# Performance work log

Hardware: AMD Instinct MI355X
Metric: run time of the kernel (lower is better)

The kernel has to match this reference:

```python
import jax, jax.numpy as jnp
import numpy as np

B, T = 65536, 100          # batch of trajectories, hard-coded 100-step unrolled loop
D_CP, D_FIN, HID, D_OUT = 2, 3, 12, 2  # control-point dim, finger dim, SimpleRNN units, Dense out


def setup_inputs() -> dict:
    key = jax.random.key(0)
    k0, k1, k2, k3, k4 = jax.random.split(key, 5)
    return {
        "control_point_input": jax.random.normal(k0, (B, T, D_CP), jnp.float32),
        "finger_input": jax.random.normal(k1, (B, T, D_FIN), jnp.float32),
        # SimpleRNN kernel / recurrent kernel / bias ('random_normal', 'zeros')
        "W_rnn": jax.random.normal(k2, (D_CP + D_FIN, HID), jnp.float32) * 0.05,
        "U_rnn": jax.random.normal(k3, (HID, HID), jnp.float32) * 0.05,
        "b_rnn": jnp.zeros((HID,), jnp.float32),
        # Dense(2) kernel / bias
        "W_out": jax.random.normal(k4, (D_CP + HID, D_OUT), jnp.float32) * 0.05,
        "b_out": jnp.zeros((D_OUT,), jnp.float32),
    }


def reference(control_point_input, finger_input, W_rnn, U_rnn, b_rnn, W_out, b_out):
    """Non-teacher-forcing branch of DeformationTrackerBiFlowModel.call.

    Keras SimpleRNN (stateful=False) is invoked on a single timestep each
    iteration, so its hidden state is reset to zero every call and the
    recurrent kernel U_rnn contributes h0 @ U_rnn == 0 (mathematically inert).
    The true autoregressive recurrence flows through the Dense(2) output fed
    back as the next step's input -> expressed with a single lax.scan.
    """
    cp0 = control_point_input[:, 0, :]                # (B, 2), reused at every step
    fin = jnp.transpose(finger_input, (1, 0, 2))      # (T, B, 3) for scan

    def step(prev_out, fin_t):
        # prev_out: (B, 2) previous predicted control point; fin_t: (B, 3)
        x = jnp.concatenate([prev_out, fin_t], axis=-1)          # (B, 5)
        h = jnp.tanh(x @ W_rnn + b_rnn)                          # (B, 12); h0 @ U_rnn == 0
        out = jnp.concatenate([cp0, h], axis=-1) @ W_out + b_out  # (B, 2)
        return out, out

    _, outs = jax.lax.scan(step, cp0, fin)            # outs: (T, B, 2)
    return jnp.transpose(outs, (1, 0, 2))             # (B, T, 2)
```

## Files before the change

kernel.cpp:

```cpp
#include <hip/hip_runtime.h>


constexpr int Bn  = 65536;
constexpr int Tn  = 100;
constexpr int HID = 12;
constexpr int LPR = 4;
constexpr int UPL = 3;

template <int CTRL>
__device__ __forceinline__ float dpp_mov(float x) {
    return __builtin_bit_cast(float,
        __builtin_amdgcn_mov_dpp(__builtin_bit_cast(int, x), CTRL, 0xF, 0xF, true));
}

__device__ __forceinline__ float fast_tanh(float a) {
    const float t = __builtin_amdgcn_exp2f(a * 2.885390081777927f);
    return __builtin_fmaf(-2.0f, __builtin_amdgcn_rcpf(1.0f + t), 1.0f);
}

__global__ __launch_bounds__(256, 4) void deform_kernel(
    const float* __restrict__ cp,
    const float* __restrict__ fin,
    const float* __restrict__ Wr,
    const float* __restrict__ br_,
    const float* __restrict__ Wo,
    const float* __restrict__ bo_,
    float* __restrict__ out)
{
    const int tid = blockIdx.x * blockDim.x + threadIdx.x;
    const int row = tid >> 2;
    const int q   = tid & 3;
    const int j0  = q * UPL;

    float w0[UPL], w1[UPL], w2[UPL], w3[UPL], w4[UPL];
    float brv[UPL], wo0[UPL], wo1[UPL];
    #pragma unroll
    for (int u = 0; u < UPL; ++u) {
        const int j = j0 + u;
        w0[u] = Wr[0 * HID + j];
        w1[u] = Wr[1 * HID + j];
        w2[u] = Wr[2 * HID + j];
        w3[u] = Wr[3 * HID + j];
        w4[u] = Wr[4 * HID + j];
        brv[u] = br_[j];
        wo0[u] = Wo[(2 + j) * 2 + 0];
        wo1[u] = Wo[(2 + j) * 2 + 1];
    }
    const float wo00 = Wo[0], wo01 = Wo[1];
    const float wo10 = Wo[2], wo11 = Wo[3];
    const float bo0 = bo_[0], bo1 = bo_[1];

    const float cp0x = cp[(size_t)row * Tn * 2 + 0];
    const float cp0y = cp[(size_t)row * Tn * 2 + 1];

    const float oc0 = bo0 + cp0x * wo00 + cp0y * wo10;
    const float oc1 = bo1 + cp0x * wo01 + cp0y * wo11;

    float px = cp0x, py = cp0y;

    const float4* __restrict__ fp = reinterpret_cast<const float4*>(fin + (size_t)row * Tn * 3);
    float2* __restrict__ op = reinterpret_cast<float2*>(out + (size_t)row * Tn * 2);

    float4 cur0 = fp[0], cur1 = fp[1], cur2 = fp[2];
    float4 nxt0 = fp[3], nxt1 = fp[4], nxt2 = fp[5];

    #pragma unroll 1
    for (int c = 0; c < 25; ++c) {
        const int cpre = (c + 2 < 25) ? (c + 2) : 24;
        const float4 pf0 = fp[cpre * 3 + 0];
        const float4 pf1 = fp[cpre * 3 + 1];
        const float4 pf2 = fp[cpre * 3 + 2];

        const float f[12] = {cur0.x, cur0.y, cur0.z, cur0.w,
                             cur1.x, cur1.y, cur1.z, cur1.w,
                             cur2.x, cur2.y, cur2.z, cur2.w};

        float so0 = 0.0f, so1 = 0.0f;
        #pragma unroll
        for (int s = 0; s < 4; ++s) {
            const float fx = f[s * 3 + 0];
            const float fy = f[s * 3 + 1];
            const float fz = f[s * 3 + 2];
            float o0p = 0.0f, o1p = 0.0f;
            #pragma unroll
            for (int u = 0; u < UPL; ++u) {
                float a = brv[u];
                a = __builtin_fmaf(px, w0[u], a);
                a = __builtin_fmaf(py, w1[u], a);
                a = __builtin_fmaf(fx, w2[u], a);
                a = __builtin_fmaf(fy, w3[u], a);
                a = __builtin_fmaf(fz, w4[u], a);
                const float h = fast_tanh(a);
                o0p = __builtin_fmaf(h, wo0[u], o0p);
                o1p = __builtin_fmaf(h, wo1[u], o1p);
            }
            o0p += dpp_mov<0xB1>(o0p);
            o1p += dpp_mov<0xB1>(o1p);
            o0p += dpp_mov<0x4E>(o0p);
            o1p += dpp_mov<0x4E>(o1p);

            const float o0 = oc0 + o0p;
            const float o1 = oc1 + o1p;
            if (q == s) { so0 = o0; so1 = o1; }
            px = o0; py = o1;
        }

        op[c * 4 + q] = make_float2(so0, so1);

        cur0 = nxt0; cur1 = nxt1; cur2 = nxt2;
        nxt0 = pf0;  nxt1 = pf1;  nxt2 = pf2;
    }
}

extern "C" void kernel_launch(void* const* d_in, const int* in_sizes, int n_in,
                              void* d_out, int out_size, void* d_ws, size_t ws_size,
                              hipStream_t stream) {
    const float* cp  = (const float*)d_in[0];
    const float* fin = (const float*)d_in[1];
    const float* Wr  = (const float*)d_in[2];
    const float* br  = (const float*)d_in[4];
    const float* Wo  = (const float*)d_in[5];
    const float* bo  = (const float*)d_in[6];
    float* out = (float*)d_out;

    const int threads = Bn * LPR;
    deform_kernel<<<dim3(threads / 256), dim3(256), 0, stream>>>(cp, fin, Wr, br, Wo, bo, out);
}
```

Baseline: 210.3 us.

## Process two trajectories per 4-lane group with interleaved recurrences and float4 stores

Each 4-lane group now advances two independent rows at once, interleaving their serial recurrence chains so the tanh/FMA/DPP latency of one row can overlap with the other. The finger-input contribution is computed ahead of the recurrent term, which shortens the dependent chain. Outputs are buffered over two chunks and written as float4 instead of float2. In exchange, register use roughly doubles, occupancy is relaxed to 2 blocks per CU, and half as many threads are launched.

```diff
diff --git a/kernel.cpp b/kernel.cpp
--- a/kernel.cpp
+++ b/kernel.cpp
@@ -4,7 +4,6 @@
 constexpr int Bn  = 65536;
 constexpr int Tn  = 100;
 constexpr int HID = 12;
-constexpr int LPR = 4;
 constexpr int UPL = 3;
 
 template <int CTRL>
@@ -18,7 +17,7 @@
     return __builtin_fmaf(-2.0f, __builtin_amdgcn_rcpf(1.0f + t), 1.0f);
 }
 
-__global__ __launch_bounds__(256, 4) void deform_kernel(
+__global__ __launch_bounds__(256, 2) void deform_kernel(
     const float* __restrict__ cp,
     const float* __restrict__ fin,
     const float* __restrict__ Wr,
@@ -27,10 +26,10 @@
     const float* __restrict__ bo_,
     float* __restrict__ out)
 {
-    const int tid = blockIdx.x * blockDim.x + threadIdx.x;
-    const int row = tid >> 2;
-    const int q   = tid & 3;
-    const int j0  = q * UPL;
+    const int tid   = blockIdx.x * blockDim.x + threadIdx.x;
+    const int group = tid >> 2;
+    const int q     = tid & 3;
+    const int j0    = q * UPL;
 
     float w0[UPL], w1[UPL], w2[UPL], w3[UPL], w4[UPL];
     float brv[UPL], wo0[UPL], wo1[UPL];
@@ -50,65 +49,115 @@
     const float wo10 = Wo[2], wo11 = Wo[3];
     const float bo0 = bo_[0], bo1 = bo_[1];
 
-    const float cp0x = cp[(size_t)row * Tn * 2 + 0];
-    const float cp0y = cp[(size_t)row * Tn * 2 + 1];
+    const int rowA = group * 2;
+    const int rowB = rowA + 1;
 
-    const float oc0 = bo0 + cp0x * wo00 + cp0y * wo10;
-    const float oc1 = bo1 + cp0x * wo01 + cp0y * wo11;
+    const float cpAx = cp[(size_t)rowA * Tn * 2 + 0];
+    const float cpAy = cp[(size_t)rowA * Tn * 2 + 1];
+    const float cpBx = cp[(size_t)rowB * Tn * 2 + 0];
+    const float cpBy = cp[(size_t)rowB * Tn * 2 + 1];
 
-    float px = cp0x, py = cp0y;
+    const float ocA0 = bo0 + cpAx * wo00 + cpAy * wo10;
+    const float ocA1 = bo1 + cpAx * wo01 + cpAy * wo11;
+    const float ocB0 = bo0 + cpBx * wo00 + cpBy * wo10;
+    const float ocB1 = bo1 + cpBx * wo01 + cpBy * wo11;
 
-    const float4* __restrict__ fp = reinterpret_cast<const float4*>(fin + (size_t)row * Tn * 3);
-    float2* __restrict__ op = reinterpret_cast<float2*>(out + (size_t)row * Tn * 2);
+    float pxA = cpAx, pyA = cpAy;
+    float pxB = cpBx, pyB = cpBy;
 
-    float4 cur0 = fp[0], cur1 = fp[1], cur2 = fp[2];
-    float4 nxt0 = fp[3], nxt1 = fp[4], nxt2 = fp[5];
+    const float4* __restrict__ fpA = reinterpret_cast<const float4*>(fin + (size_t)rowA * Tn * 3);
+    const float4* __restrict__ fpB = reinterpret_cast<const float4*>(fin + (size_t)rowB * Tn * 3);
+    float4* __restrict__ o4A = reinterpret_cast<float4*>(out) + (size_t)rowA * 50;
+    float4* __restrict__ o4B = reinterpret_cast<float4*>(out) + (size_t)rowB * 50;
+
+    float4 cA0 = fpA[0], cA1 = fpA[1], cA2 = fpA[2];
+    float4 nA0 = fpA[3], nA1 = fpA[4], nA2 = fpA[5];
+    float4 cB0 = fpB[0], cB1 = fpB[1], cB2 = fpB[2];
+    float4 nB0 = fpB[3], nB1 = fpB[4], nB2 = fpB[5];
+
+    float4 vA = make_float4(0.f, 0.f, 0.f, 0.f);
+    float4 vB = make_float4(0.f, 0.f, 0.f, 0.f);
 
     #pragma unroll 1
     for (int c = 0; c < 25; ++c) {
         const int cpre = (c + 2 < 25) ? (c + 2) : 24;
-        const float4 pf0 = fp[cpre * 3 + 0];
-        const float4 pf1 = fp[cpre * 3 + 1];
-        const float4 pf2 = fp[cpre * 3 + 2];
+        const float4 pA0 = fpA[cpre * 3 + 0];
+        const float4 pA1 = fpA[cpre * 3 + 1];
+        const float4 pA2 = fpA[cpre * 3 + 2];
+        const float4 pB0 = fpB[cpre * 3 + 0];
+        const float4 pB1 = fpB[cpre * 3 + 1];
+        const float4 pB2 = fpB[cpre * 3 + 2];
 
-        const float f[12] = {cur0.x, cur0.y, cur0.z, cur0.w,
-                             cur1.x, cur1.y, cur1.z, cur1.w,
-                             cur2.x, cur2.y, cur2.z, cur2.w};
+        const float fA[12] = {cA0.x, cA0.y, cA0.z, cA0.w,
+                              cA1.x, cA1.y, cA1.z, cA1.w,
+                              cA2.x, cA2.y, cA2.z, cA2.w};
+        const float fB[12] = {cB0.x, cB0.y, cB0.z, cB0.w,
+                              cB1.x, cB1.y, cB1.z, cB1.w,
+                              cB2.x, cB2.y, cB2.z, cB2.w};
 
-        float so0 = 0.0f, so1 = 0.0f;
+        const int par = c & 1;
         #pragma unroll
         for (int s = 0; s < 4; ++s) {
-            const float fx = f[s * 3 + 0];
-            const float fy = f[s * 3 + 1];
-            const float fz = f[s * 3 + 2];
-            float o0p = 0.0f, o1p = 0.0f;
+            const float fAx = fA[s * 3 + 0], fAy = fA[s * 3 + 1], fAz = fA[s * 3 + 2];
+            const float fBx = fB[s * 3 + 0], fBy = fB[s * 3 + 1], fBz = fB[s * 3 + 2];
+
+            float oA0 = 0.0f, oA1 = 0.0f, oB0 = 0.0f, oB1 = 0.0f;
             #pragma unroll
             for (int u = 0; u < UPL; ++u) {
-                float a = brv[u];
-                a = __builtin_fmaf(px, w0[u], a);
-                a = __builtin_fmaf(py, w1[u], a);
-                a = __builtin_fmaf(fx, w2[u], a);
-                a = __builtin_fmaf(fy, w3[u], a);
-                a = __builtin_fmaf(fz, w4[u], a);
-                const float h = fast_tanh(a);
-                o0p = __builtin_fmaf(h, wo0[u], o0p);
-                o1p = __builtin_fmaf(h, wo1[u], o1p);
+                const float gA = __builtin_fmaf(fAz, w4[u],
+                                 __builtin_fmaf(fAy, w3[u],
+                                 __builtin_fmaf(fAx, w2[u], brv[u])));
+                const float gB = __builtin_fmaf(fBz, w4[u],
+                                 __builtin_fmaf(fBy, w3[u],
+                                 __builtin_fmaf(fBx, w2[u], brv[u])));
+                const float aA = __builtin_fmaf(pyA, w1[u],
+                                 __builtin_fmaf(pxA, w0[u], gA));
+                const float aB = __builtin_fmaf(pyB, w1[u],
+                                 __builtin_fmaf(pxB, w0[u], gB));
+                const float hA = fast_tanh(aA);
+                const float hB = fast_tanh(aB);
+                oA0 = __builtin_fmaf(hA, wo0[u], oA0);
+                oA1 = __builtin_fmaf(hA, wo1[u], oA1);
+                oB0 = __builtin_fmaf(hB, wo0[u], oB0);
+                oB1 = __builtin_fmaf(hB, wo1[u], oB1);
             }
-            o0p += dpp_mov<0xB1>(o0p);
-            o1p += dpp_mov<0xB1>(o1p);
-            o0p += dpp_mov<0x4E>(o0p);
-            o1p += dpp_mov<0x4E>(o1p);
+            oA0 += dpp_mov<0xB1>(oA0);
+            oA1 += dpp_mov<0xB1>(oA1);
+            oB0 += dpp_mov<0xB1>(oB0);
+            oB1 += dpp_mov<0xB1>(oB1);
+            oA0 += dpp_mov<0x4E>(oA0);
+            oA1 += dpp_mov<0x4E>(oA1);
+            oB0 += dpp_mov<0x4E>(oB0);
+            oB1 += dpp_mov<0x4E>(oB1);
 
-            const float o0 = oc0 + o0p;
-            const float o1 = oc1 + o1p;
-            if (q == s) { so0 = o0; so1 = o1; }
-            px = o0; py = o1;
+            const float outA0 = ocA0 + oA0, outA1 = ocA1 + oA1;
+            const float outB0 = ocB0 + oB0, outB1 = ocB1 + oB1;
+
+            if (q == 2 * par + (s >> 1)) {
+                if ((s & 1) == 0) { vA.x = outA0; vA.y = outA1;
+                                    vB.x = outB0; vB.y = outB1; }
+                else              { vA.z = outA0; vA.w = outA1;
+                                    vB.z = outB0; vB.w = outB1; }
+            }
+            pxA = outA0; pyA = outA1;
+            pxB = outB0; pyB = outB1;
         }
 
-        op[c * 4 + q] = make_float2(so0, so1);
+        if (par) {
+            const int m = c >> 1;
+            o4A[m * 4 + q] = vA;
+            o4B[m * 4 + q] = vB;
+        }
 
-        cur0 = nxt0; cur1 = nxt1; cur2 = nxt2;
-        nxt0 = pf0;  nxt1 = pf1;  nxt2 = pf2;
+        cA0 = nA0; cA1 = nA1; cA2 = nA2;
+        nA0 = pA0; nA1 = pA1; nA2 = pA2;
+        cB0 = nB0; cB1 = nB1; cB2 = nB2;
+        nB0 = pB0; nB1 = pB1; nB2 = pB2;
+    }
+
+    if (q < 2) {
+        o4A[48 + q] = vA;
+        o4B[48 + q] = vB;
     }
 }
 
@@ -123,6 +172,6 @@
     const float* bo  = (const float*)d_in[6];
     float* out = (float*)d_out;
 
-    const int threads = Bn * LPR;
+    const int threads = (Bn / 2) * 4;
     deform_kernel<<<dim3(threads / 256), dim3(256), 0, stream>>>(cp, fin, Wr, br, Wo, bo, out);
 }
```

Result: faster. 204.9 us (-2.6%).
